# Kernel optimization log

Hardware: AMD Instinct MI355X
Metric: run time of the kernel (lower is better)

Reference implementation:

```python
import jax, jax.numpy as jnp
import numpy as np

MODES = 32
WIDTH = 64


def crelu(z):
    # split-complex ReLU (torch.relu is undefined on complex; this is the standard fix)
    return jax.nn.relu(z.real) + 1j * jax.nn.relu(z.imag)


def _linear_params(key, fan_in, fan_out):
    k1, k2 = jax.random.split(key)
    s = 1.0 / np.sqrt(fan_in)
    W = jax.random.uniform(k1, (fan_out, fan_in), minval=-s, maxval=s, dtype=jnp.float32)
    b = jax.random.uniform(k2, (fan_out,), minval=-s, maxval=s, dtype=jnp.float32)
    return W, b


def setup_inputs() -> dict:
    key = jax.random.key(0)
    ks = jax.random.split(key, 8)
    B, G = 32768, 512
    H0, H1, H2 = 1024, 512, 64  # hidden_layers; H2 == WIDTH
    FD = 128                    # field_dim
    geometry_input = jax.random.normal(ks[0], (B, G), dtype=jnp.float32)
    W_in, b_in = _linear_params(ks[1], G, H0)
    W_h1, b_h1 = _linear_params(ks[2], H0, H1)
    W_h2, b_h2 = _linear_params(ks[3], H1, H2)
    w0 = jax.random.normal(ks[4], (MODES, WIDTH), dtype=jnp.float32)
    w1 = jax.random.normal(ks[5], (MODES, WIDTH), dtype=jnp.float32)
    lin1_W, lin1_b = _linear_params(ks[6], WIDTH, WIDTH)
    k7a, k7b = jax.random.split(ks[7])
    lin2_W, lin2_b = _linear_params(k7a, WIDTH, WIDTH)
    W_out, b_out = _linear_params(k7b, H2, FD)
    return dict(geometry_input=geometry_input, W_in=W_in, b_in=b_in,
                W_h1=W_h1, b_h1=b_h1, W_h2=W_h2, b_h2=b_h2,
                w0=w0, w1=w1, lin1_W=lin1_W, lin1_b=lin1_b,
                lin2_W=lin2_W, lin2_b=lin2_b, W_out=W_out, b_out=b_out)


def reference(geometry_input, W_in, b_in, W_h1, b_h1, W_h2, b_h2,
              w0, w1, lin1_W, lin1_b, lin2_W, lin2_b, W_out, b_out):
    # MLP encoder: [B, G] -> [B, 64]
    x = jax.nn.relu(geometry_input @ W_in.T + b_in)
    x = jax.nn.relu(x @ W_h1.T + b_h1)
    x = jax.nn.relu(x @ W_h2.T + b_h2)
    # FNO block
    xh = jnp.fft.fftn(x)  # fftn over ALL axes, as in torch code -> complex64 [B, 64]
    phase = jnp.exp(1j * 2.0 * jnp.pi * jnp.arange(MODES) / MODES).astype(jnp.complex64)
    y = xh[:, None, :] * w0  # per-mode lift: [B, MODES, WIDTH]
    y = crelu(y)
    y = y * phase[None, :, None]  # diagonal L mode-multiply
    y = jnp.einsum('bmw,mw->bw', y, w1.astype(y.dtype))  # collapse modes -> [B, WIDTH]
    y = crelu(y @ lin1_W.T + lin1_b)  # real weights on complex acts
    y = y @ lin2_W.T + lin2_b
    y = jnp.fft.ifftn(y)  # [B, 64] complex
    out = y @ W_out.T + b_out  # [B, field_dim] complex
    return out
```

## Files before the change

### kernel.cpp

```cpp
#include <hip/hip_runtime.h>
#include <hip/hip_bf16.h>


#define PI2F 6.28318530717958647692f

typedef __attribute__((ext_vector_type(8))) short short8;
typedef __attribute__((ext_vector_type(4))) float f32x4;

__device__ __forceinline__ unsigned short f2bf(float f) {
  unsigned int u = __float_as_uint(f);
  u += 0x7fff + ((u >> 16) & 1);
  return (unsigned short)(u >> 16);
}
__device__ __forceinline__ unsigned int pack_bf16x2(float a, float b) {
  return (unsigned int)f2bf(a) | ((unsigned int)f2bf(b) << 16);
}

__device__ __forceinline__ void gl2lds16(const void* gptr, const void* lptr) {
  __builtin_amdgcn_global_load_lds(
      (const __attribute__((address_space(1))) unsigned int*)(unsigned long long)gptr,
      (__attribute__((address_space(3))) unsigned int*)(unsigned int)(unsigned long long)lptr,
      16, 0, 0);
}

__global__ __launch_bounds__(256) void f32_to_bf16_k(
    const float* __restrict__ src, unsigned short* __restrict__ dst, int n4)
{
  int i = blockIdx.x * 256 + threadIdx.x;
  if (i < n4) {
    float4 v = ((const float4*)src)[i];
    uint2 p;
    p.x = pack_bf16x2(v.x, v.y);
    p.y = pack_bf16x2(v.z, v.w);
    ((uint2*)dst)[i] = p;
  }
}

template<int NBLOG, typename OUT>
__global__ __launch_bounds__(512, 1) void gemm_pipe(
    const unsigned short* __restrict__ A, const unsigned short* __restrict__ Bw,
    const float* __restrict__ bias, OUT* __restrict__ C, int N, int K)
{
  constexpr int BM = 128, BN = 256, BK = 64;
  constexpr int ASZ = BM * BK;
  constexpr int BSZ = BN * BK;
  constexpr int BUF = ASZ + BSZ;
  __shared__ __align__(16) unsigned short lds[3 * BUF];

  const int nwg = gridDim.x;
  const int cpx = nwg >> 3;
  const int orig = blockIdx.x;
  const int wg = (orig & 7) * cpx + (orig >> 3);
  const int mb = wg >> NBLOG;
  const int nb = wg & ((1 << NBLOG) - 1);
  const size_t m0 = (size_t)mb * BM;
  const size_t n0 = (size_t)nb * BN;

  const int tid = threadIdx.x;
  const int lane = tid & 63;
  const int wv = tid >> 6;
  const int q = lane >> 4, lr = lane & 15;
  const int x7 = lr & 7;
  const int wm = (wv >> 2) * 64;
  const int wn = (wv & 3) * 64;
  f32x4 acc[4][4] = {};

  auto STAGE_HALF = [&](int r, int kk, int s0) {
    unsigned short* dA = lds + r * BUF;
    #pragma unroll
    for (int u = 0; u < 3; ++u) {
      int e = wv * 6 + s0 + u;
      int isA = (e < 16) ? 1 : 0;
      int e2 = isA ? e : e - 16;
      int pc = e2 * 64 + lane;
      int row = pc >> 3, col = pc & 7;
      int lc = col ^ (row & 7);
      const unsigned short* src = isA ? A : Bw;
      size_t rb = isA ? m0 : n0;
      unsigned short* dst = dA + (isA ? 0 : ASZ) + e2 * 512;
      gl2lds16(src + (rb + row) * (size_t)K + kk + lc * 8, dst);
    }
  };

  const int nt = K / BK;
  STAGE_HALF(0, 0, 0); STAGE_HALF(0, 0, 3);
  STAGE_HALF(1, BK, 0); STAGE_HALF(1, BK, 3);
  asm volatile("s_waitcnt vmcnt(6)" ::: "memory");
  __builtin_amdgcn_s_barrier();

  int r0 = 0;
  for (int t = 0; t < nt; ++t) {
    const unsigned short* sA = lds + r0 * BUF;
    const unsigned short* sB = sA + ASZ;
    const bool st = (t + 2) < nt;
    const int r2 = (r0 >= 1) ? (r0 - 1) : 2;
    const int kk2 = (t + 2) * BK;

    short8 af[4][2], bf0[2][2];
    #pragma unroll
    for (int i = 0; i < 4; ++i)
      #pragma unroll
      for (int t2 = 0; t2 < 2; ++t2)
        af[i][t2] = *(const short8*)(sA + (wm + i * 16 + lr) * 64 + (((t2 << 2) | q) ^ x7) * 8);
    #pragma unroll
    for (int j = 0; j < 2; ++j)
      #pragma unroll
      for (int t2 = 0; t2 < 2; ++t2)
        bf0[j][t2] = *(const short8*)(sB + (wn + j * 16 + lr) * 64 + (((t2 << 2) | q) ^ x7) * 8);
    if (st) STAGE_HALF(r2, kk2, 0);
    __builtin_amdgcn_s_setprio(1);
    #pragma unroll
    for (int i = 0; i < 4; ++i)
      #pragma unroll
      for (int j = 0; j < 2; ++j)
        #pragma unroll
        for (int t2 = 0; t2 < 2; ++t2)
          acc[i][j] = __builtin_amdgcn_mfma_f32_16x16x32_bf16(af[i][t2], bf0[j][t2], acc[i][j], 0, 0, 0);
    __builtin_amdgcn_s_setprio(0);
    __builtin_amdgcn_s_barrier();

    short8 bf1[2][2];
    #pragma unroll
    for (int j = 0; j < 2; ++j)
      #pragma unroll
      for (int t2 = 0; t2 < 2; ++t2)
        bf1[j][t2] = *(const short8*)(sB + (wn + (j + 2) * 16 + lr) * 64 + (((t2 << 2) | q) ^ x7) * 8);
    if (st) STAGE_HALF(r2, kk2, 3);
    __builtin_amdgcn_s_setprio(1);
    #pragma unroll
    for (int i = 0; i < 4; ++i)
      #pragma unroll
      for (int j = 0; j < 2; ++j)
        #pragma unroll
        for (int t2 = 0; t2 < 2; ++t2)
          acc[i][j + 2] = __builtin_amdgcn_mfma_f32_16x16x32_bf16(af[i][t2], bf1[j][t2], acc[i][j + 2], 0, 0, 0);
    __builtin_amdgcn_s_setprio(0);

    asm volatile("s_waitcnt lgkmcnt(0)" ::: "memory");
    if (st) { asm volatile("s_waitcnt vmcnt(6)" ::: "memory"); }
    else    { asm volatile("s_waitcnt vmcnt(0)" ::: "memory"); }
    __builtin_amdgcn_s_barrier();
    r0 = (r0 + 1 >= 3) ? 0 : r0 + 1;
  }

  #pragma unroll
  for (int i = 0; i < 4; ++i)
    #pragma unroll
    for (int j = 0; j < 4; ++j) {
      size_t col = n0 + wn + j * 16 + lr;
      float bv = bias[col];
      #pragma unroll
      for (int r = 0; r < 4; ++r) {
        size_t row = m0 + wm + i * 16 + q * 4 + r;
        float v = acc[i][j][r] + bv;
        v = v > 0.f ? v : 0.f;
        if (sizeof(OUT) == 2) ((unsigned short*)C)[row * N + col] = f2bf(v);
        else                  ((float*)C)[row * N + col] = v;
      }
    }
}

template<int BM, int BN, int WM, int WN, typename OUT>
__global__ __launch_bounds__(256) void gemm_async(
    const unsigned short* __restrict__ A, const unsigned short* __restrict__ Bw,
    const float* __restrict__ bias, OUT* __restrict__ C,
    int M, int N, int K)
{
  constexpr int BK = 64;
  __shared__ __align__(16) unsigned short lA[BM * BK];
  __shared__ __align__(16) unsigned short lB[BN * BK];
  const int tid = threadIdx.x;
  const int lane = tid & 63;
  const int wv = tid >> 6;
  const int q = lane >> 4, lr = lane & 15;
  const int x7 = lr & 7;
  constexpr int WN_CNT = BN / WN;
  const int wm = (wv / WN_CNT) * WM;
  const int wn = (wv % WN_CNT) * WN;
  const size_t m0 = (size_t)blockIdx.x * BM;
  const size_t n0 = (size_t)blockIdx.y * BN;
  constexpr int MI = WM / 16, NI = WN / 16;
  f32x4 acc[MI][NI] = {};
  constexpr int A_INSTR = BM * BK / 512;
  constexpr int B_INSTR = BN * BK / 512;
  constexpr int A_PW = A_INSTR / 4, B_PW = B_INSTR / 4;
  (void)M;

  for (int k0 = 0; k0 < K; k0 += BK) {
    __syncthreads();
    #pragma unroll
    for (int s = 0; s < A_PW; ++s) {
      int instr = wv * A_PW + s;
      int pc = instr * 64 + lane;
      int row = pc >> 3, col = pc & 7;
      int lc = col ^ (row & 7);
      gl2lds16(A + (m0 + row) * K + k0 + lc * 8, lA + instr * 512);
    }
    #pragma unroll
    for (int s = 0; s < B_PW; ++s) {
      int instr = wv * B_PW + s;
      int pc = instr * 64 + lane;
      int row = pc >> 3, col = pc & 7;
      int lc = col ^ (row & 7);
      gl2lds16(Bw + (n0 + row) * K + k0 + lc * 8, lB + instr * 512);
    }
    __syncthreads();
    #pragma unroll
    for (int t = 0; t < 2; ++t) {
      short8 af[MI], bfr[NI];
      #pragma unroll
      for (int i = 0; i < MI; ++i) {
        int r = wm + i * 16 + lr;
        af[i] = *(const short8*)(lA + r * 64 + (((t << 2) | q) ^ x7) * 8);
      }
      #pragma unroll
      for (int j = 0; j < NI; ++j) {
        int r = wn + j * 16 + lr;
        bfr[j] = *(const short8*)(lB + r * 64 + (((t << 2) | q) ^ x7) * 8);
      }
      #pragma unroll
      for (int i = 0; i < MI; ++i)
        #pragma unroll
        for (int j = 0; j < NI; ++j)
          acc[i][j] = __builtin_amdgcn_mfma_f32_16x16x32_bf16(af[i], bfr[j], acc[i][j], 0, 0, 0);
    }
  }
  #pragma unroll
  for (int i = 0; i < MI; ++i)
    #pragma unroll
    for (int j = 0; j < NI; ++j) {
      size_t col = n0 + wn + j * 16 + lr;
      float bv = bias[col];
      #pragma unroll
      for (int r = 0; r < 4; ++r) {
        size_t row = m0 + wm + i * 16 + q * 4 + r;
        float v = acc[i][j][r] + bv;
        v = v > 0.f ? v : 0.f;
        if (sizeof(OUT) == 2) ((unsigned short*)C)[row * N + col] = f2bf(v);
        else                  ((float*)C)[row * N + col] = v;
      }
    }
}

__global__ __launch_bounds__(256) void precompute(
    const float* __restrict__ w0, const float* __restrict__ w1,
    const float* __restrict__ l2W, const float* __restrict__ l2b,
    float2* __restrict__ Ap, float2* __restrict__ Am,
    float2* __restrict__ Qt, float2* __restrict__ b2c)
{
  const int t = threadIdx.x;
  const int blk = blockIdx.x;
  if (blk == 0) {
    if (t < 64) {
      float apx = 0, apy = 0, amx = 0, amy = 0;
      for (int m = 0; m < 32; ++m) {
        float s0 = w0[m * 64 + t];
        float cf = w1[m * 64 + t] * s0;
        float sn, cs; sincosf(PI2F * (float)m / 32.f, &sn, &cs);
        if (s0 > 0.f)      { apx += cs * cf; apy += sn * cf; }
        else if (s0 < 0.f) { amx += cs * cf; amy += sn * cf; }
      }
      Ap[t] = make_float2(apx, apy);
      Am[t] = make_float2(amx, amy);
      float bx = 0, by = 0;
      for (int k = 0; k < 64; ++k) {
        float sn, cs; sincosf(PI2F * (float)((t * k) & 63) / 64.f, &sn, &cs);
        float lb = l2b[k] * (1.f / 64.f);
        bx += cs * lb; by += sn * lb;
      }
      b2c[t] = make_float2(bx, by);
    }
  } else {
    int e = (blk - 1) * 256 + t;
    int j = e >> 6, w = e & 63;
    float qx = 0, qy = 0;
    for (int k = 0; k < 64; ++k) {
      float sn, cs; sincosf(PI2F * (float)((j * k) & 63) / 64.f, &sn, &cs);
      float lw = l2W[k * 64 + w] * (1.f / 64.f);
      qx += cs * lw; qy += sn * lw;
    }
    Qt[w * 64 + j] = make_float2(qx, qy);
  }
}

__global__ __launch_bounds__(256) void dft64_rows(
    const float* __restrict__ x3, float2* __restrict__ xh1)
{
  __shared__ __align__(16) float xt[32][64];
  __shared__ float2 tw[64];
  const int t = threadIdx.x;
  const size_t b0 = (size_t)blockIdx.x * 32;
  for (int it = 0; it < 8; ++it) {
    int idx = it * 256 + t;
    int r = idx >> 6, w = idx & 63;
    xt[r][w] = x3[(b0 + r) * 64 + w];
  }
  if (t < 64) {
    float sn, cs; sincosf(-PI2F * (float)t / 64.f, &sn, &cs);
    tw[t] = make_float2(cs, sn);
  }
  __syncthreads();
  const int k = t & 63, rg = t >> 6;
  float2 acc[8] = {};
  #pragma unroll 1
  for (int w4 = 0; w4 < 16; ++w4) {
    int w = 4 * w4;
    int kw = k * w;
    float2 t0 = tw[kw & 63];
    float2 t1 = tw[(kw + k) & 63];
    float2 t2 = tw[(kw + 2 * k) & 63];
    float2 t3 = tw[(kw + 3 * k) & 63];
    #pragma unroll
    for (int r = 0; r < 8; ++r) {
      float4 xv = *(const float4*)(&xt[rg * 8 + r][w]);
      acc[r].x += xv.x * t0.x + xv.y * t1.x + xv.z * t2.x + xv.w * t3.x;
      acc[r].y += xv.x * t0.y + xv.y * t1.y + xv.z * t2.y + xv.w * t3.y;
    }
  }
  #pragma unroll
  for (int r = 0; r < 8; ++r)
    xh1[(b0 + rg * 8 + r) * 64 + k] = acc[r];
}

template<int SIGN>
__global__ __launch_bounds__(256) void fft_stage1(
    const float2* __restrict__ Xin, float2* __restrict__ T)
{
  __shared__ float2 tile[128 * 33];
  __shared__ float2 tw16s[16];
  const int blk = blockIdx.x;
  const int b2 = blk >> 1, wh = (blk & 1) * 32;
  const int t = threadIdx.x;
  for (int it = 0; it < 16; ++it) {
    int idx = it * 256 + t;
    int b1 = idx >> 5, wi = idx & 31;
    tile[b1 * 33 + wi] = Xin[((size_t)(b1 * 256 + b2)) * 64 + wh + wi];
  }
  if (t < 16) {
    float sn, cs; sincosf(SIGN * PI2F * (float)t / 16.f, &sn, &cs);
    tw16s[t] = make_float2(cs, sn);
  }
  __syncthreads();
  const int p = t >> 1, n2a = p >> 4, k1pa = p & 15, w0 = (t & 1) * 16;
  float2 ya[16] = {};
  #pragma unroll 1
  for (int n1 = 0; n1 < 16; ++n1) {
    float2 tv = tw16s[(n1 * k1pa) & 15];
    const float2* row = &tile[(8 * n1 + n2a) * 33 + w0];
    #pragma unroll
    for (int w = 0; w < 16; ++w) {
      float2 d = row[w];
      ya[w].x += d.x * tv.x - d.y * tv.y;
      ya[w].y += d.x * tv.y + d.y * tv.x;
    }
  }
  {
    float sn, cs; sincosf(SIGN * PI2F * (float)(n2a * k1pa) / 128.f, &sn, &cs);
    #pragma unroll
    for (int w = 0; w < 16; ++w) {
      float2 a = ya[w];
      ya[w] = make_float2(a.x * cs - a.y * sn, a.x * sn + a.y * cs);
    }
  }
  __syncthreads();
  {
    float2* yrow = &tile[(n2a * 16 + k1pa) * 33 + w0];
    #pragma unroll
    for (int w = 0; w < 16; ++w) yrow[w] = ya[w];
  }
  __syncthreads();
  const int wB = t & 31, qB = t >> 5;
  float sstep, cstep;
  sincosf(SIGN * PI2F * (float)(16 * b2) / 32768.f, &sstep, &cstep);
  #pragma unroll 1
  for (int h = 0; h < 2; ++h) {
    const int k1p = qB + 8 * h;
    float2 acc[8] = {};
    #pragma unroll 1
    for (int n2 = 0; n2 < 8; ++n2) {
      float2 d = tile[(n2 * 16 + k1p) * 33 + wB];
      #pragma unroll
      for (int k2p = 0; k2p < 8; ++k2p) {
        float2 tv = tw16s[(2 * n2 * k2p) & 15];
        acc[k2p].x += d.x * tv.x - d.y * tv.y;
        acc[k2p].y += d.x * tv.y + d.y * tv.x;
      }
    }
    float sb, cb;
    sincosf(SIGN * PI2F * (float)(b2 * k1p) / 32768.f, &sb, &cb);
    float2 rot = make_float2(cb, sb);
    #pragma unroll
    for (int k2p = 0; k2p < 8; ++k2p) {
      int k1 = k1p + 16 * k2p;
      float2 a = acc[k2p];
      float2 o = make_float2(a.x * rot.x - a.y * rot.y,
                             a.x * rot.y + a.y * rot.x);
      T[((size_t)k1 * 256 + b2) * 64 + wh + wB] = o;
      float nrx = rot.x * cstep - rot.y * sstep;
      rot.y = rot.x * sstep + rot.y * cstep;
      rot.x = nrx;
    }
  }
}

template<int SIGN, bool SCALE>
__global__ __launch_bounds__(256) void fft_stage2(
    const float2* __restrict__ T, float2* __restrict__ X)
{
  __shared__ float2 tile[256 * 17];
  __shared__ float2 tw16s[16];
  const int blk = blockIdx.x;
  const int k1 = blk >> 2, wq = (blk & 3) * 16;
  const int t = threadIdx.x;
  for (int it = 0; it < 16; ++it) {
    int idx = it * 256 + t;
    int r2 = idx >> 4, wi = idx & 15;
    tile[r2 * 17 + wi] = T[((size_t)k1 * 256 + r2) * 64 + wq + wi];
  }
  if (t < 16) {
    float sn, cs; sincosf(SIGN * PI2F * (float)t / 16.f, &sn, &cs);
    tw16s[t] = make_float2(cs, sn);
  }
  __syncthreads();
  const int n2a = t >> 4, k1pa = t & 15;
  float2 ya[16] = {};
  #pragma unroll 1
  for (int n1 = 0; n1 < 16; ++n1) {
    float2 tv = tw16s[(n1 * k1pa) & 15];
    const float2* row = &tile[(16 * n1 + n2a) * 17];
    #pragma unroll
    for (int w = 0; w < 16; ++w) {
      float2 d = row[w];
      ya[w].x += d.x * tv.x - d.y * tv.y;
      ya[w].y += d.x * tv.y + d.y * tv.x;
    }
  }
  {
    float sn, cs; sincosf(SIGN * PI2F * (float)(n2a * k1pa) / 256.f, &sn, &cs);
    #pragma unroll
    for (int w = 0; w < 16; ++w) {
      float2 a = ya[w];
      ya[w] = make_float2(a.x * cs - a.y * sn, a.x * sn + a.y * cs);
    }
  }
  __syncthreads();
  {
    float2* yrow = &tile[(n2a * 16 + k1pa) * 17];
    #pragma unroll
    for (int w = 0; w < 16; ++w) yrow[w] = ya[w];
  }
  __syncthreads();
  const int k1pb = t >> 4, wB = t & 15;
  float2 acc[16] = {};
  #pragma unroll 1
  for (int n2 = 0; n2 < 16; ++n2) {
    float2 d = tile[(n2 * 16 + k1pb) * 17 + wB];
    #pragma unroll
    for (int k2p = 0; k2p < 16; ++k2p) {
      float2 tv = tw16s[(n2 * k2p) & 15];
      acc[k2p].x += d.x * tv.x - d.y * tv.y;
      acc[k2p].y += d.x * tv.y + d.y * tv.x;
    }
  }
  const float sc = SCALE ? (1.f / 32768.f) : 1.f;
  #pragma unroll
  for (int k2p = 0; k2p < 16; ++k2p) {
    int k2 = k1pb + 16 * k2p;
    size_t row = (size_t)(k1 + 128 * k2);
    X[row * 64 + wq + wB] = make_float2(acc[k2p].x * sc, acc[k2p].y * sc);
  }
}

__global__ __launch_bounds__(256) void pw_lin(
    const float2* __restrict__ xh,
    const float2* __restrict__ Ap, const float2* __restrict__ Am,
    const float* __restrict__ l1W, const float* __restrict__ l1b,
    const float2* __restrict__ Qt, const float2* __restrict__ b2c,
    float2* __restrict__ u)
{
  __shared__ __align__(16) float2 tile[32][64];
  __shared__ __align__(16) float2 qt[64 * 64];
  const int t = threadIdx.x;
  const int lane = t & 63;
  const int wv = t >> 6;
  const size_t b0 = (size_t)blockIdx.x * 32;

  #pragma unroll
  for (int s = 0; s < 8; ++s) {
    int instr = wv * 8 + s;
    gl2lds16((const char*)Qt + instr * 1024 + lane * 16,
             (const char*)qt + instr * 1024);
  }

  for (int it = 0; it < 8; ++it) {
    int idx = it * 256 + t;
    int r = idx >> 6, w = idx & 63;
    float2 xv = xh[(b0 + r) * 64 + w];
    float2 Aa = (xv.x >= 0.f) ? Ap[w] : Am[w];
    float2 Ab = (xv.y >= 0.f) ? Ap[w] : Am[w];
    tile[r][w] = make_float2(xv.x * Aa.x - xv.y * Ab.y,
                             xv.x * Aa.y + xv.y * Ab.x);
  }
  __syncthreads();

  const int n = lane, rg = wv;

  {
    float2 acc[8] = {};
    const float* wrow = l1W + n * 64;
    float4 lwn = *(const float4*)wrow;
    #pragma unroll 1
    for (int w2 = 0; w2 < 16; ++w2) {
      float4 lw = lwn;
      lwn = *(const float4*)(wrow + 4 * ((w2 + 1) & 15));
      int w = 4 * w2;
      #pragma unroll
      for (int r = 0; r < 8; ++r) {
        const float4* rowp = (const float4*)(&tile[rg * 8 + r][w]);
        float4 y01 = rowp[0];
        float4 y23 = rowp[1];
        acc[r].x += y01.x * lw.x + y01.z * lw.y + y23.x * lw.z + y23.z * lw.w;
        acc[r].y += y01.y * lw.x + y01.w * lw.y + y23.y * lw.z + y23.w * lw.w;
      }
    }
    float bb = l1b[n];
    #pragma unroll
    for (int r = 0; r < 8; ++r) {
      float zr = acc[r].x + bb; zr = zr > 0.f ? zr : 0.f;
      float zi = acc[r].y;      zi = zi > 0.f ? zi : 0.f;
      tile[rg * 8 + r][n] = make_float2(zr, zi);
    }
  }

  {
    const int j = lane;
    float2 acc[8] = {};
    #pragma unroll 1
    for (int w2 = 0; w2 < 16; ++w2) {
      int w = 4 * w2;
      float2 q0 = qt[(w + 0) * 64 + j];
      float2 q1 = qt[(w + 1) * 64 + j];
      float2 q2 = qt[(w + 2) * 64 + j];
      float2 q3 = qt[(w + 3) * 64 + j];
      #pragma unroll
      for (int r = 0; r < 8; ++r) {
        const float4* rowp = (const float4*)(&tile[rg * 8 + r][w]);
        float4 z01 = rowp[0];
        float4 z23 = rowp[1];
        acc[r].x += z01.x * q0.x - z01.y * q0.y
                  + z01.z * q1.x - z01.w * q1.y
                  + z23.x * q2.x - z23.y * q2.y
                  + z23.z * q3.x - z23.w * q3.y;
        acc[r].y += z01.x * q0.y + z01.y * q0.x
                  + z01.z * q1.y + z01.w * q1.x
                  + z23.x * q2.y + z23.y * q2.x
                  + z23.z * q3.y + z23.w * q3.x;
      }
    }
    float2 bc = b2c[j];
    #pragma unroll
    for (int r = 0; r < 8; ++r)
      u[(b0 + rg * 8 + r) * 64 + j] = make_float2(acc[r].x + bc.x, acc[r].y + bc.y);
  }
}

template<int MODE>
__global__ __launch_bounds__(256) void final_out(
    const float2* __restrict__ v, const float* __restrict__ Wout,
    const float* __restrict__ bout, float* __restrict__ out)
{
  __shared__ __align__(16) float2 vt[32][64];
  const int t = threadIdx.x;
  const size_t b0 = (size_t)blockIdx.x * 32;
  for (int it = 0; it < 8; ++it) {
    int idx = it * 256 + t;
    int r = idx >> 6, w = idx & 63;
    vt[r][w] = v[(b0 + r) * 64 + w];
  }
  __syncthreads();
  const int f = t & 127, rg = t >> 7;
  const float* wrow = Wout + f * 64;
  float2 acc[16] = {};
  float2 wvn = *(const float2*)wrow;
  #pragma unroll 1
  for (int j2 = 0; j2 < 32; ++j2) {
    float2 wc = wvn;
    wvn = *(const float2*)(wrow + 2 * ((j2 + 1) & 31));
    #pragma unroll
    for (int r = 0; r < 16; ++r) {
      float4 vv = *(const float4*)(&vt[rg * 16 + r][2 * j2]);
      acc[r].x += vv.x * wc.x + vv.z * wc.y;
      acc[r].y += vv.y * wc.x + vv.w * wc.y;
    }
  }
  float bb = bout[f];
  #pragma unroll
  for (int r = 0; r < 16; ++r) {
    size_t idx = (b0 + rg * 16 + r) * 128 + f;
    if (MODE == 0) out[idx] = acc[r].x + bb;
    else ((float2*)out)[idx] = make_float2(acc[r].x + bb, acc[r].y);
  }
}

extern "C" void kernel_launch(void* const* d_in, const int* in_sizes, int n_in,
                              void* d_out, int out_size, void* d_ws, size_t ws_size,
                              hipStream_t stream)
{
  (void)in_sizes; (void)n_in; (void)ws_size;
  const float* geom = (const float*)d_in[0];
  const float* Win  = (const float*)d_in[1];
  const float* bin  = (const float*)d_in[2];
  const float* Wh1  = (const float*)d_in[3];
  const float* bh1  = (const float*)d_in[4];
  const float* Wh2  = (const float*)d_in[5];
  const float* bh2  = (const float*)d_in[6];
  const float* w0   = (const float*)d_in[7];
  const float* w1   = (const float*)d_in[8];
  const float* l1W  = (const float*)d_in[9];
  const float* l1b  = (const float*)d_in[10];
  const float* l2W  = (const float*)d_in[11];
  const float* l2b  = (const float*)d_in[12];
  const float* Wout = (const float*)d_in[13];
  const float* bout = (const float*)d_in[14];

  char* ws = (char*)d_ws;
  const size_t MB = 1048576ull;
  unsigned short* geomb = (unsigned short*)(ws);
  unsigned short* x2b   = (unsigned short*)(ws);
  unsigned short* x1b   = (unsigned short*)(ws + 32 * MB);
  float*  x3  = (float*)(ws + 32 * MB);
  float2* S0  = (float2*)(ws + 40 * MB);
  float2* S1  = (float2*)(ws + 56 * MB);
  float2* Ap  = (float2*)(ws + 72 * MB);
  float2* Am  = (float2*)(ws + 72 * MB + 512);
  float2* b2c = (float2*)(ws + 72 * MB + 1024);
  float2* Qt  = (float2*)(ws + 72 * MB + 1536);
  unsigned short* Winb = (unsigned short*)(ws + 96 * MB);
  unsigned short* Wh1b = (unsigned short*)(ws + 97 * MB);
  unsigned short* Wh2b = (unsigned short*)(ws + 98 * MB);

  f32_to_bf16_k<<<16384, 256, 0, stream>>>(geom, geomb, 4194304);
  f32_to_bf16_k<<<512, 256, 0, stream>>>(Win, Winb, 131072);
  f32_to_bf16_k<<<512, 256, 0, stream>>>(Wh1, Wh1b, 131072);
  f32_to_bf16_k<<<32, 256, 0, stream>>>(Wh2, Wh2b, 8192);

  gemm_pipe<2, unsigned short><<<1024, 512, 0, stream>>>(
      geomb, Winb, bin, x1b, 1024, 512);
  gemm_pipe<1, unsigned short><<<512, 512, 0, stream>>>(
      x1b, Wh1b, bh1, x2b, 512, 1024);
  gemm_async<128, 64,64,32,float><<<dim3(256, 1), 256, 0, stream>>>(
      x2b, Wh2b, bh2, x3, 32768, 64, 512);

  precompute<<<17, 256, 0, stream>>>(w0, w1, l2W, l2b, Ap, Am, Qt, b2c);
  dft64_rows<<<1024, 256, 0, stream>>>(x3, S0);
  fft_stage1<-1><<<512, 256, 0, stream>>>(S0, S1);
  fft_stage2<-1, false><<<512, 256, 0, stream>>>(S1, S0);
  pw_lin<<<1024, 256, 0, stream>>>(S0, Ap, Am, l1W, l1b, Qt, b2c, S1);
  fft_stage1<1><<<512, 256, 0, stream>>>(S1, S0);
  fft_stage2<1, true><<<512, 256, 0, stream>>>(S0, S1);
  if (out_size >= 8388608) {
    final_out<1><<<1024, 256, 0, stream>>>(S1, Wout, bout, (float*)d_out);
  } else {
    final_out<0><<<1024, 256, 0, stream>>>(S1, Wout, bout, (float*)d_out);
  }
}
```

Measured before the change: 443.5 us.

## Restructure FFT stage DFTs into register-resident small DFTs with vectorized loads

Both FFT stage kernels now load their tiles with float4 global loads into a padded, 16-byte-aligned LDS layout. The first-pass DFT is reorganised so each thread keeps a full 16-point column in registers and computes all outputs from it. Twiddles are cached in registers and per-element sincos is replaced by a rotation recurrence. The goal is fewer LDS reads, fewer bank conflicts and cheaper twiddle work in the FFT stages, at the cost of higher register pressure and slightly different rounding from the recurrence.

```diff
diff --git a/kernel.cpp b/kernel.cpp
--- a/kernel.cpp
+++ b/kernel.cpp
@@ -326,65 +326,84 @@
 __global__ __launch_bounds__(256) void fft_stage1(
     const float2* __restrict__ Xin, float2* __restrict__ T)
 {
-  __shared__ float2 tile[128 * 33];
+  __shared__ __align__(16) float2 tile[128 * 34];
   __shared__ float2 tw16s[16];
   const int blk = blockIdx.x;
   const int b2 = blk >> 1, wh = (blk & 1) * 32;
   const int t = threadIdx.x;
-  for (int it = 0; it < 16; ++it) {
+  #pragma unroll
+  for (int it = 0; it < 8; ++it) {
     int idx = it * 256 + t;
-    int b1 = idx >> 5, wi = idx & 31;
-    tile[b1 * 33 + wi] = Xin[((size_t)(b1 * 256 + b2)) * 64 + wh + wi];
+    int b1 = idx >> 4, wi = (idx & 15) * 2;
+    float4 v = *(const float4*)&Xin[((size_t)(b1 * 256 + b2)) * 64 + wh + wi];
+    *(float4*)&tile[b1 * 34 + wi] = v;
   }
   if (t < 16) {
     float sn, cs; sincosf(SIGN * PI2F * (float)t / 16.f, &sn, &cs);
     tw16s[t] = make_float2(cs, sn);
   }
   __syncthreads();
-  const int p = t >> 1, n2a = p >> 4, k1pa = p & 15, w0 = (t & 1) * 16;
-  float2 ya[16] = {};
-  #pragma unroll 1
-  for (int n1 = 0; n1 < 16; ++n1) {
-    float2 tv = tw16s[(n1 * k1pa) & 15];
-    const float2* row = &tile[(8 * n1 + n2a) * 33 + w0];
-    #pragma unroll
-    for (int w = 0; w < 16; ++w) {
-      float2 d = row[w];
-      ya[w].x += d.x * tv.x - d.y * tv.y;
-      ya[w].y += d.x * tv.y + d.y * tv.x;
-    }
-  }
+  float2 twr[16];
+  #pragma unroll
+  for (int j = 0; j < 16; ++j) twr[j] = tw16s[j];
+
   {
-    float sn, cs; sincosf(SIGN * PI2F * (float)(n2a * k1pa) / 128.f, &sn, &cs);
-    #pragma unroll
-    for (int w = 0; w < 16; ++w) {
-      float2 a = ya[w];
-      ya[w] = make_float2(a.x * cs - a.y * sn, a.x * sn + a.y * cs);
-    }
+    const int n2a = t >> 5, w = t & 31;
+    float2 d[16];
+    #pragma unroll
+    for (int n1 = 0; n1 < 16; ++n1)
+      d[n1] = tile[(8 * n1 + n2a) * 34 + w];
+    float2 y[16];
+    #pragma unroll
+    for (int k = 0; k < 16; ++k) {
+      float2 a = d[0];
+      #pragma unroll
+      for (int n1 = 1; n1 < 16; ++n1) {
+        float2 tv = twr[(n1 * k) & 15];
+        a.x += d[n1].x * tv.x - d[n1].y * tv.y;
+        a.y += d[n1].x * tv.y + d[n1].y * tv.x;
+      }
+      y[k] = a;
+    }
+    float sstep, cstep;
+    sincosf(SIGN * PI2F * (float)n2a / 128.f, &sstep, &cstep);
+    float2 rot = make_float2(1.f, 0.f);
+    #pragma unroll
+    for (int k = 0; k < 16; ++k) {
+      float2 a = y[k];
+      y[k] = make_float2(a.x * rot.x - a.y * rot.y, a.x * rot.y + a.y * rot.x);
+      float nrx = rot.x * cstep - rot.y * sstep;
+      rot.y = rot.x * sstep + rot.y * cstep;
+      rot.x = nrx;
+    }
+    __syncthreads();
+    #pragma unroll
+    for (int k = 0; k < 16; ++k)
+      tile[(n2a * 16 + k) * 34 + w] = y[k];
   }
   __syncthreads();
-  {
-    float2* yrow = &tile[(n2a * 16 + k1pa) * 33 + w0];
-    #pragma unroll
-    for (int w = 0; w < 16; ++w) yrow[w] = ya[w];
-  }
-  __syncthreads();
+
   const int wB = t & 31, qB = t >> 5;
   float sstep, cstep;
   sincosf(SIGN * PI2F * (float)(16 * b2) / 32768.f, &sstep, &cstep);
-  #pragma unroll 1
+  #pragma unroll
   for (int h = 0; h < 2; ++h) {
     const int k1p = qB + 8 * h;
-    float2 acc[8] = {};
-    #pragma unroll 1
-    for (int n2 = 0; n2 < 8; ++n2) {
-      float2 d = tile[(n2 * 16 + k1p) * 33 + wB];
-      #pragma unroll
-      for (int k2p = 0; k2p < 8; ++k2p) {
-        float2 tv = tw16s[(2 * n2 * k2p) & 15];
-        acc[k2p].x += d.x * tv.x - d.y * tv.y;
-        acc[k2p].y += d.x * tv.y + d.y * tv.x;
-      }
+    float2 d[8];
+    #pragma unroll
+    for (int n2 = 0; n2 < 8; ++n2)
+      d[n2] = tile[(n2 * 16 + k1p) * 34 + wB];
+    float2 acc[8];
+    #pragma unroll
+    for (int k2p = 0; k2p < 8; ++k2p) {
+      float2 a = d[0];
+      #pragma unroll
+      for (int n2 = 1; n2 < 8; ++n2) {
+        float2 tv = twr[(2 * n2 * k2p) & 15];
+        a.x += d[n2].x * tv.x - d[n2].y * tv.y;
+        a.y += d[n2].x * tv.y + d[n2].y * tv.x;
+      }
+      acc[k2p] = a;
     }
     float sb, cb;
     sincosf(SIGN * PI2F * (float)(b2 * k1p) / 32768.f, &sb, &cb);
@@ -393,9 +412,8 @@
     for (int k2p = 0; k2p < 8; ++k2p) {
       int k1 = k1p + 16 * k2p;
       float2 a = acc[k2p];
-      float2 o = make_float2(a.x * rot.x - a.y * rot.y,
-                             a.x * rot.y + a.y * rot.x);
-      T[((size_t)k1 * 256 + b2) * 64 + wh + wB] = o;
+      T[((size_t)k1 * 256 + b2) * 64 + wh + wB] =
+          make_float2(a.x * rot.x - a.y * rot.y, a.x * rot.y + a.y * rot.x);
       float nrx = rot.x * cstep - rot.y * sstep;
       rot.y = rot.x * sstep + rot.y * cstep;
       rot.x = nrx;
@@ -407,67 +425,81 @@
 __global__ __launch_bounds__(256) void fft_stage2(
     const float2* __restrict__ T, float2* __restrict__ X)
 {
-  __shared__ float2 tile[256 * 17];
+  __shared__ __align__(16) float2 tile[256 * 18];
   __shared__ float2 tw16s[16];
   const int blk = blockIdx.x;
   const int k1 = blk >> 2, wq = (blk & 3) * 16;
   const int t = threadIdx.x;
-  for (int it = 0; it < 16; ++it) {
+  #pragma unroll
+  for (int it = 0; it < 8; ++it) {
     int idx = it * 256 + t;
-    int r2 = idx >> 4, wi = idx & 15;
-    tile[r2 * 17 + wi] = T[((size_t)k1 * 256 + r2) * 64 + wq + wi];
+    int r2 = idx >> 3, wi = (idx & 7) * 2;
+    float4 v = *(const float4*)&T[((size_t)k1 * 256 + r2) * 64 + wq + wi];
+    *(float4*)&tile[r2 * 18 + wi] = v;
   }
   if (t < 16) {
     float sn, cs; sincosf(SIGN * PI2F * (float)t / 16.f, &sn, &cs);
     tw16s[t] = make_float2(cs, sn);
   }
   __syncthreads();
-  const int n2a = t >> 4, k1pa = t & 15;
-  float2 ya[16] = {};
-  #pragma unroll 1
-  for (int n1 = 0; n1 < 16; ++n1) {
-    float2 tv = tw16s[(n1 * k1pa) & 15];
-    const float2* row = &tile[(16 * n1 + n2a) * 17];
-    #pragma unroll
-    for (int w = 0; w < 16; ++w) {
-      float2 d = row[w];
-      ya[w].x += d.x * tv.x - d.y * tv.y;
-      ya[w].y += d.x * tv.y + d.y * tv.x;
-    }
-  }
+  float2 twr[16];
+  #pragma unroll
+  for (int j = 0; j < 16; ++j) twr[j] = tw16s[j];
+
   {
-    float sn, cs; sincosf(SIGN * PI2F * (float)(n2a * k1pa) / 256.f, &sn, &cs);
-    #pragma unroll
-    for (int w = 0; w < 16; ++w) {
-      float2 a = ya[w];
-      ya[w] = make_float2(a.x * cs - a.y * sn, a.x * sn + a.y * cs);
-    }
+    const int n2a = t >> 4, w = t & 15;
+    float2 d[16];
+    #pragma unroll
+    for (int n1 = 0; n1 < 16; ++n1)
+      d[n1] = tile[(16 * n1 + n2a) * 18 + w];
+    float2 y[16];
+    #pragma unroll
+    for (int k = 0; k < 16; ++k) {
+      float2 a = d[0];
+      #pragma unroll
+      for (int n1 = 1; n1 < 16; ++n1) {
+        float2 tv = twr[(n1 * k) & 15];
+        a.x += d[n1].x * tv.x - d[n1].y * tv.y;
+        a.y += d[n1].x * tv.y + d[n1].y * tv.x;
+      }
+      y[k] = a;
+    }
+    float sstep, cstep;
+    sincosf(SIGN * PI2F * (float)n2a / 256.f, &sstep, &cstep);
+    float2 rot = make_float2(1.f, 0.f);
+    #pragma unroll
+    for (int k = 0; k < 16; ++k) {
+      float2 a = y[k];
+      y[k] = make_float2(a.x * rot.x - a.y * rot.y, a.x * rot.y + a.y * rot.x);
+      float nrx = rot.x * cstep - rot.y * sstep;
+      rot.y = rot.x * sstep + rot.y * cstep;
+      rot.x = nrx;
+    }
+    __syncthreads();
+    #pragma unroll
+    for (int k = 0; k < 16; ++k)
+      tile[(n2a * 16 + k) * 18 + w] = y[k];
   }
   __syncthreads();
-  {
-    float2* yrow = &tile[(n2a * 16 + k1pa) * 17];
-    #pragma unroll
-    for (int w = 0; w < 16; ++w) yrow[w] = ya[w];
-  }
-  __syncthreads();
+
   const int k1pb = t >> 4, wB = t & 15;
-  float2 acc[16] = {};
-  #pragma unroll 1
-  for (int n2 = 0; n2 < 16; ++n2) {
-    float2 d = tile[(n2 * 16 + k1pb) * 17 + wB];
-    #pragma unroll
-    for (int k2p = 0; k2p < 16; ++k2p) {
-      float2 tv = tw16s[(n2 * k2p) & 15];
-      acc[k2p].x += d.x * tv.x - d.y * tv.y;
-      acc[k2p].y += d.x * tv.y + d.y * tv.x;
-    }
-  }
+  float2 d[16];
+  #pragma unroll
+  for (int n2 = 0; n2 < 16; ++n2)
+    d[n2] = tile[(n2 * 16 + k1pb) * 18 + wB];
   const float sc = SCALE ? (1.f / 32768.f) : 1.f;
   #pragma unroll
   for (int k2p = 0; k2p < 16; ++k2p) {
+    float2 a = d[0];
+    #pragma unroll
+    for (int n2 = 1; n2 < 16; ++n2) {
+      float2 tv = twr[(n2 * k2p) & 15];
+      a.x += d[n2].x * tv.x - d[n2].y * tv.y;
+      a.y += d[n2].x * tv.y + d[n2].y * tv.x;
+    }
     int k2 = k1pb + 16 * k2p;
     size_t row = (size_t)(k1 + 128 * k2);
-    X[row * 64 + wq + wB] = make_float2(acc[k2p].x * sc, acc[k2p].y * sc);
+    X[row * 64 + wq + wB] = make_float2(a.x * sc, a.y * sc);
   }
 }
 
```

After: 414.9 us. 1.07x faster.
